# Kernel optimization log

Hardware: AMD Instinct MI355X
Metric: run time of the kernel (lower is better)

Reference implementation:

```python
import jax, jax.numpy as jnp
import numpy as np

HEADS = 6
K = 3       # kernel_size
PAD = 1     # padding (stride = 1, so AvgPool is identity and h=H, w=W)


def setup_inputs() -> dict:
    key = jax.random.key(0)
    ks = jax.random.split(key, 6)
    B, H, W, C = 8, 56, 56, 192
    k4h = (K ** 4) * HEADS  # 486
    s = 0.02
    return {
        "x":  jax.random.normal(ks[0], (B, H, W, C), jnp.float32),
        # weights stored as (in, out), i.e. transpose of torch nn.Linear.weight
        "Wv": jax.random.normal(ks[1], (C, C), jnp.float32) * s,
        "Wa": jax.random.normal(ks[2], (C, k4h), jnp.float32) * s,
        "ba": jnp.zeros((k4h,), jnp.float32),
        "Wp": jax.random.normal(ks[3], (C, C), jnp.float32) * s,
        "bp": jnp.zeros((C,), jnp.float32),
    }


def _outlook(x, Wv, Wa, ba, Wp, bp):
    B, H, W, C = x.shape
    hd = C // HEADS
    scale = hd ** (-0.5)
    k2 = K * K
    hw = H * W

    # v projection (no bias), to NCHW
    v = jnp.einsum("bhwc,cd->bdhw", x, Wv)                       # [B,C,H,W]

    # unfold: extract k x k local windows (same ordering as nn.Unfold: C, ki, kj)
    vp = jnp.pad(v, ((0, 0), (0, 0), (PAD, PAD), (PAD, PAD)))
    patches = jnp.stack(
        [vp[:, :, i:i + H, j:j + W] for i in range(K) for j in range(K)],
        axis=2,
    )                                                            # [B,C,k2,H,W]
    v = patches.reshape(B, HEADS, hd, k2, hw).transpose(0, 1, 4, 3, 2)  # [B,h,hw,k2,hd]

    # attention weights: dense predicted per location (pool is identity, stride=1)
    a = x.reshape(B, hw, C) @ Wa + ba                            # [B,hw,heads*k2*k2]
    a = a.reshape(B, hw, HEADS, k2, k2).transpose(0, 2, 1, 3, 4)  # [B,h,hw,k2,k2]
    a = jax.nn.softmax(a * scale, axis=-1)

    out = jnp.einsum("bnpkq,bnpqd->bnpkd", a, v)                 # [B,h,hw,k2,hd]

    # fold (col2im): scatter-add overlapping windows back, stride=1
    cols = out.transpose(0, 1, 4, 3, 2).reshape(B, C, K, K, H, W)
    acc = jnp.zeros((B, C, H + 2 * PAD, W + 2 * PAD), x.dtype)
    for i in range(K):
        for j in range(K):
            acc = acc.at[:, :, i:i + H, j:j + W].add(cols[:, :, i, j])
    y = acc[:, :, PAD:PAD + H, PAD:PAD + W].transpose(0, 2, 3, 1)  # [B,H,W,C]

    return y @ Wp + bp


def reference(x, Wv, Wa, ba, Wp, bp):
    return _outlook(x, Wv, Wa, ba, Wp, bp)
```

## Files before the change

### kernel.cpp

```cpp
#include <hip/hip_runtime.h>
#include <hip/hip_bf16.h>
#include <cstdint>

#define DI __device__ __forceinline__

typedef __attribute__((ext_vector_type(8))) short short8;
typedef __attribute__((ext_vector_type(4))) float f32x4;

DI float bflo(uint32_t u) { return __builtin_bit_cast(float, (uint32_t)(u << 16)); }
DI float bfhi(uint32_t u) { return __builtin_bit_cast(float, (uint32_t)(u & 0xffff0000u)); }
DI uint32_t cvtpk(float lo, float hi) {
    uint32_t r;
    asm("v_cvt_pk_bf16_f32 %0, %1, %2" : "=v"(r) : "v"(lo), "v"(hi));
    return r;
}
#if __has_builtin(__builtin_amdgcn_cvt_pk_fp8_f32)
DI uint32_t fp8pk(float a, float b) {
    return (uint32_t)__builtin_amdgcn_cvt_pk_fp8_f32(a, b, 0, false);
}
#else
DI uint32_t fp8pk(float a, float b) {
    uint32_t r;
    asm("v_cvt_pk_fp8_f32 %0, %1, %2" : "=v"(r) : "v"(a), "v"(b));
    return r;
}
#endif
#if __has_builtin(__builtin_amdgcn_cvt_f32_fp8)
#define FP8DEC(dw, sel) __builtin_amdgcn_cvt_f32_fp8((dw), (sel))
#else
DI float fp8dec_(uint32_t dw, int sel) {
    const uint32_t u = (dw >> (8 * sel)) & 0xFFu;
    const uint32_t s = (u & 0x80u) << 24;
    const uint32_t em = u & 0x7Fu;
    float mag;
    if (em >= 8) mag = __builtin_bit_cast(float, (((em >> 3) + 120u) << 23) | ((em & 7u) << 20));
    else         mag = (float)em * 0.001953125f;
    return __builtin_bit_cast(float, s | __builtin_bit_cast(uint32_t, mag));
}
#define FP8DEC(dw, sel) fp8dec_((dw), (sel))
#endif
DI void gload16(const void* g, void* s) {
    __builtin_amdgcn_global_load_lds(
        (const __attribute__((address_space(1))) uint32_t*)g,
        (__attribute__((address_space(3))) uint32_t*)s, 16, 0, 0);
}
DI int xcd_swizzle(int orig, int nwg) {
    const int q = nwg >> 3, r = nwg & 7;
    const int x = orig & 7, i = orig >> 3;
    return (x < r ? x * (q + 1) : r * (q + 1) + (x - r) * q) + i;
}

constexpr int BATCH = 8, HH_IMG = 56, WW_IMG = 56, C = 192;
constexpr int HEADS = 6, HD = 32, NA = 486;
constexpr int NAPB = 576;
constexpr int HSTA = 96;
constexpr int MROWS = BATCH * HH_IMG * WW_IMG;
constexpr int KK = 192;
constexpr int TILE_B  = 49152;
constexpr int PANEL_B = 49152;
constexpr int WTB_B   = 73728;

__global__ __launch_bounds__(256) void prep_all(const float* __restrict__ x,
                                                const float* __restrict__ Wv,
                                                const float* __restrict__ Wa,
                                                const float* __restrict__ Wp,
                                                const float* __restrict__ ba,
                                                uint8_t* __restrict__ xbf,
                                                uint8_t* __restrict__ WT,
                                                uint8_t* __restrict__ WTB,
                                                float* __restrict__ baP) {
    const int bid = blockIdx.x;
    if (bid < 2352) {
        const int g = bid * 256 + threadIdx.x;
        const int m = g / 24, cc = g % 24;
        const int ks = cc >> 2, lg = cc & 3;
        const float* src = x + (size_t)m * KK + cc * 8;
        const float4 v0 = *(const float4*)src;
        const float4 v1 = *(const float4*)(src + 4);
        uint4 o;
        o.x = cvtpk(v0.x, v0.y); o.y = cvtpk(v0.z, v0.w);
        o.z = cvtpk(v1.x, v1.y); o.w = cvtpk(v1.z, v1.w);
        const size_t off = (size_t)(m >> 7) * PANEL_B +
                           ((((m >> 4) & 7) * 6 + ks) * 64 + (lg << 4) + (m & 15)) * 16;
        *(uint4*)(xbf + off) = o;
        return;
    }
    const int tid = (bid - 2352) * 256 + threadIdx.x;
    if (tid < 18432) {
        const int s = tid % 24, rem = tid / 24;
        const int p = rem & 127, tile = rem >> 7;
        const int lc = (p >> 5) * 32 + 2 * (p & 15) + ((p >> 4) & 1);
        const int u  = tile * 128 + lc;
        const float* src = nullptr; int nc = 0, col = 0;
        if (u < 192) { src = Wv; nc = 192; col = u; }
        else {
            const int up = u - 192;
            const int head = up / HSTA, r96 = up - head * HSTA;
            if (r96 < 81) { src = Wa; nc = NA; col = head * 81 + r96; }
        }
        const int k0 = s * 8;
        uint32_t d[4];
#pragma unroll
        for (int e = 0; e < 4; ++e) {
            const float f0 = src ? src[(size_t)(k0 + 2 * e) * nc + col]     : 0.f;
            const float f1 = src ? src[(size_t)(k0 + 2 * e + 1) * nc + col] : 0.f;
            d[e] = cvtpk(f0, f1);
        }
        const int sb = (s * 16) ^ ((p & 7) << 4);
        *(uint4*)(WT + (size_t)tile * TILE_B + p * 384 + sb) =
            make_uint4(d[0], d[1], d[2], d[3]);
    } else if (tid < 18432 + 4608) {
        const int g = tid - 18432;
        const int l = g & 63, gg = g >> 6;
        const int ks = gg % 6, nrIdx = gg / 6;
        const int pp = nrIdx >> 1, h = nrIdx & 1;
        const int col = pp * 32 + 2 * (l & 15) + h;
        const int k0  = ks * 32 + (l >> 4) * 8;
        uint32_t d[4];
#pragma unroll
        for (int e = 0; e < 4; ++e) {
            const float f0 = Wp[(size_t)(k0 + 2 * e) * 192 + col];
            const float f1 = Wp[(size_t)(k0 + 2 * e + 1) * 192 + col];
            d[e] = cvtpk(f0, f1);
        }
        *(uint4*)(WTB + (size_t)g * 16) = make_uint4(d[0], d[1], d[2], d[3]);
    } else if (tid < 18432 + 4608 + NAPB) {
        const int pc = tid - 18432 - 4608;
        const int head = pc / HSTA, r96 = pc - head * HSTA;
        baP[pc] = (r96 < 81) ? ba[head * 81 + r96] : 0.f;
    }
}

__global__ __launch_bounds__(256, 2) void gemm_fr(
    const uint8_t* __restrict__ Afr,
    const uint8_t* __restrict__ WT,
    uint16_t* __restrict__ zOut, uint8_t* __restrict__ alogP,
    const float* __restrict__ baP) {
    __shared__ __align__(16) uint8_t sm[TILE_B];
    const int t    = threadIdx.x;
    const int wgid = xcd_swizzle(blockIdx.x, gridDim.x);
    const int mg   = wgid / 6, ti = wgid - mg * 6;
    const int m0   = mg * 128;
    const int l    = t & 63, wid = t >> 6;
    const int wr   = wid >> 1, wc = wid & 1;
    const int lr   = l & 15, lg = l >> 4;

    const uint8_t* wt = WT + (size_t)ti * TILE_B;
#pragma unroll
    for (int i = 0; i < 12; ++i) {
        const int off = wid * 12288 + i * 1024;
        gload16(wt + off + l * 16, sm + off);
    }

    const uint8_t* ap = Afr + (size_t)mg * PANEL_B;
    short8 aR[6][4];
#pragma unroll
    for (int ks = 0; ks < 6; ++ks)
#pragma unroll
        for (int mr = 0; mr < 4; ++mr) {
            const int r = wr * 4 + mr;
            aR[ks][mr] = *(const short8*)(ap + (size_t)(((r * 6 + ks) * 64) + l) * 16);
        }
    __syncthreads();

    f32x4 acc[4][4];
#pragma unroll
    for (int mr = 0; mr < 4; ++mr)
#pragma unroll
        for (int nr = 0; nr < 4; ++nr) acc[mr][nr] = f32x4{0.f, 0.f, 0.f, 0.f};
#pragma unroll
    for (int ks = 0; ks < 6; ++ks) {
        const int cb = ks * 64 + lg * 16;
        short8 b[4];
#pragma unroll
        for (int nr = 0; nr < 4; ++nr) {
            const int rn = wc * 64 + nr * 16 + lr;
            b[nr] = *(const short8*)(sm + rn * 384 + (cb ^ ((rn & 7) << 4)));
        }
#pragma unroll
        for (int mr = 0; mr < 4; ++mr)
#pragma unroll
            for (int nr = 0; nr < 4; ++nr)
                acc[mr][nr] = __builtin_amdgcn_mfma_f32_16x16x32_bf16(
                    aR[ks][mr], b[nr], acc[mr][nr], 0, 0, 0);
    }

    const int gcol0 = ti * 128 + wc * 64;
#pragma unroll
    for (int pr = 0; pr < 2; ++pr) {
        const int uc = gcol0 + pr * 32 + 2 * lr;
        if (uc < 192) {
#pragma unroll
            for (int mr = 0; mr < 4; ++mr) {
                const size_t rb = (size_t)(m0 + wr * 64 + mr * 16 + lg * 4);
#pragma unroll
                for (int j = 0; j < 4; ++j)
                    *(uint32_t*)(zOut + (rb + j) * 192 + uc) =
                        cvtpk(acc[mr][2 * pr][j], acc[mr][2 * pr + 1][j]);
            }
        } else {
            const int pc = uc - 192;
            const float be = baP[pc], bo = baP[pc + 1];
#pragma unroll
            for (int mr = 0; mr < 4; ++mr) {
                const size_t rb = (size_t)(m0 + wr * 64 + mr * 16 + lg * 4);
#pragma unroll
                for (int j = 0; j < 4; ++j)
                    *(uint16_t*)(alogP + (rb + j) * NAPB + pc) =
                        (uint16_t)fp8pk(acc[mr][2 * pr][j] + be,
                                        acc[mr][2 * pr + 1][j] + bo);
            }
        }
    }
}

constexpr int TH = 4, TW = 8;
constexpr int HALO_W = TW + 4;
constexpr int HSTR = 80;
constexpr int PXSTR = HEADS * HSTR;
constexpr int VL_BYTES = 96 * PXSTR;

template <int I, int J>
DI void wincoef(const uint8_t* __restrict__ rp, float (&cw)[5][5]) {
    constexpr int OFF = (I * 3 + J) * 9, A0 = OFF & ~15, BASE = OFF - A0;
    const uint4 u0 = *(const uint4*)(rp + A0);
    const uint4 u1 = *(const uint4*)(rp + A0 + 16);
    const uint32_t dd[8] = {u0.x, u0.y, u0.z, u0.w, u1.x, u1.y, u1.z, u1.w};
    constexpr float scl2 = 0.17677669529663687f * 1.4426950408889634f;
    float w[9], s = 0.f;
#define DECQ(Q) w[Q] = __builtin_amdgcn_exp2f(                                 \
        FP8DEC(dd[(BASE + Q) >> 2], (BASE + Q) & 3) * scl2); s += w[Q];
    DECQ(0) DECQ(1) DECQ(2) DECQ(3) DECQ(4) DECQ(5) DECQ(6) DECQ(7) DECQ(8)
#undef DECQ
    const float inv = __builtin_amdgcn_rcpf(s);
#pragma unroll
    for (int qi = 0; qi < 3; ++qi)
#pragma unroll
        for (int qj = 0; qj < 3; ++qj)
            cw[qi - I + 2][qj - J + 2] += w[qi * 3 + qj] * inv;
}

__global__ __launch_bounds__(192) void attn_fused(const uint16_t* __restrict__ z,
                                                  const uint8_t* __restrict__ alogP,
                                                  const uint8_t* __restrict__ WTB,
                                                  const float* __restrict__ bp,
                                                  float* __restrict__ out) {
    __shared__ __align__(16) uint8_t smem[VL_BYTES];
    const int b   = blockIdx.z;
    const int ty0 = blockIdx.y * TH, tx0 = blockIdx.x * TW;
    const int t   = threadIdx.x;

#pragma unroll
    for (int it = 0; it < 12; ++it) {
        const int f  = t + it * 192;
        const int px = f / 24, c8 = f % 24;
        const int hy = px / HALO_W, hx = px % HALO_W;
        const int y = ty0 + hy - 2, x = tx0 + hx - 2;
        uint4 val = make_uint4(0u, 0u, 0u, 0u);
        if ((unsigned)y < HH_IMG && (unsigned)x < WW_IMG)
            val = *(const uint4*)&z[(((size_t)b * HH_IMG + y) * WW_IMG + x) * C + c8 * 8];
        *(uint4*)(smem + px * PXSTR + (c8 >> 2) * HSTR + (c8 & 3) * 16) = val;
    }

    const int n   = t % HEADS, pxl = t / HEADS;
    const int py  = pxl >> 3, px_ = pxl & 7;
    const int Py  = ty0 + py, Px = tx0 + px_;

    float cw[5][5] = {};
#define WINCALL(I_, J_)                                                        \
    {                                                                          \
        const int sy = Py - I_ + 1, sx = Px - J_ + 1;                          \
        if ((unsigned)sy < HH_IMG && (unsigned)sx < WW_IMG)                    \
            wincoef<I_, J_>(alogP +                                            \
                (((size_t)b * HH_IMG + sy) * WW_IMG + sx) * NAPB + n * HSTA,   \
                cw);                                                           \
    }
    WINCALL(0, 0) WINCALL(0, 1) WINCALL(0, 2)
    WINCALL(1, 0) WINCALL(1, 1) WINCALL(1, 2)
    WINCALL(2, 0) WINCALL(2, 1) WINCALL(2, 2)
#undef WINCALL
    __syncthreads();

    float acc[HD] = {};
#pragma unroll
    for (int dy = 0; dy < 5; ++dy)
#pragma unroll
        for (int dx = 0; dx < 5; ++dx) {
            const float wq = cw[dy][dx];
            const uint8_t* vp = smem + ((py + dy) * HALO_W + (px_ + dx)) * PXSTR + n * HSTR;
#pragma unroll
            for (int v8 = 0; v8 < 4; ++v8) {
                const uint4 raw = *(const uint4*)(vp + v8 * 16);
                const uint32_t r0 = raw.x, r1 = raw.y, r2 = raw.z, r3 = raw.w;
                acc[v8*8+0] = fmaf(wq, bflo(r0), acc[v8*8+0]);
                acc[v8*8+1] = fmaf(wq, bfhi(r0), acc[v8*8+1]);
                acc[v8*8+2] = fmaf(wq, bflo(r1), acc[v8*8+2]);
                acc[v8*8+3] = fmaf(wq, bfhi(r1), acc[v8*8+3]);
                acc[v8*8+4] = fmaf(wq, bflo(r2), acc[v8*8+4]);
                acc[v8*8+5] = fmaf(wq, bfhi(r2), acc[v8*8+5]);
                acc[v8*8+6] = fmaf(wq, bflo(r3), acc[v8*8+6]);
                acc[v8*8+7] = fmaf(wq, bfhi(r3), acc[v8*8+7]);
            }
        }
    __syncthreads();

    {
        uint8_t* pb = smem + pxl * 384;
        const int key = (pxl & 7) << 4;
#pragma unroll
        for (int g2 = 0; g2 < 4; ++g2) {
            uint4 o;
            o.x = cvtpk(acc[g2 * 8 + 0], acc[g2 * 8 + 1]);
            o.y = cvtpk(acc[g2 * 8 + 2], acc[g2 * 8 + 3]);
            o.z = cvtpk(acc[g2 * 8 + 4], acc[g2 * 8 + 5]);
            o.w = cvtpk(acc[g2 * 8 + 6], acc[g2 * 8 + 7]);
            *(uint4*)(pb + ((n * 64 + g2 * 16) ^ key)) = o;
        }
    }
    __syncthreads();

    const int l = t & 63, wid = t >> 6;
    const int lr = l & 15, lg = l >> 4;
    short8 aF[2][6];
#pragma unroll
    for (int r = 0; r < 2; ++r)
#pragma unroll
        for (int ks = 0; ks < 6; ++ks) {
            const int row = r * 16 + lr;
            aF[r][ks] = *(const short8*)(smem + row * 384 +
                          ((ks * 64 + lg * 16) ^ ((row & 7) << 4)));
        }
    f32x4 gacc[2][4];
#pragma unroll
    for (int r = 0; r < 2; ++r)
#pragma unroll
        for (int f = 0; f < 4; ++f) gacc[r][f] = f32x4{0.f, 0.f, 0.f, 0.f};
#pragma unroll
    for (int ks = 0; ks < 6; ++ks) {
        short8 bF[4];
#pragma unroll
        for (int f = 0; f < 4; ++f) {
            const int nrIdx = wid * 4 + f;
            bF[f] = *(const short8*)(WTB + (size_t)(((nrIdx * 6 + ks) * 64) + l) * 16);
        }
#pragma unroll
        for (int r = 0; r < 2; ++r)
#pragma unroll
            for (int f = 0; f < 4; ++f)
                gacc[r][f] = __builtin_amdgcn_mfma_f32_16x16x32_bf16(
                    aF[r][ks], bF[f], gacc[r][f], 0, 0, 0);
    }

#pragma unroll
    for (int pi = 0; pi < 2; ++pi) {
        const int col = wid * 64 + pi * 32 + 2 * lr;
        const float be = bp[col], bo = bp[col + 1];
#pragma unroll
        for (int r = 0; r < 2; ++r)
#pragma unroll
            for (int j = 0; j < 4; ++j) {
                const int prow = r * 16 + lg * 4 + j;
                const int gy = ty0 + (prow >> 3), gx = tx0 + (prow & 7);
                float* op = out + (((size_t)b * HH_IMG + gy) * WW_IMG + gx) * C + col;
                *(float2*)op = make_float2(gacc[r][2 * pi][j] + be,
                                           gacc[r][2 * pi + 1][j] + bo);
            }
    }
}

extern "C" void kernel_launch(void* const* d_in, const int* in_sizes, int n_in,
                              void* d_out, int out_size, void* d_ws, size_t ws_size,
                              hipStream_t stream) {
    const float* x  = (const float*)d_in[0];
    const float* Wv = (const float*)d_in[1];
    const float* Wa = (const float*)d_in[2];
    const float* ba = (const float*)d_in[3];
    const float* Wp = (const float*)d_in[4];
    const float* bp = (const float*)d_in[5];
    float* out = (float*)d_out;

    uint16_t* z     = (uint16_t*)d_ws;
    uint8_t*  alogP = (uint8_t*)(z + (size_t)MROWS * C);
    uint8_t*  xbf   = alogP + (size_t)MROWS * NAPB;
    uint8_t*  WT    = xbf + (size_t)(MROWS / 128) * PANEL_B;
    uint8_t*  WTB   = WT + 6 * (size_t)TILE_B;
    float*    baP   = (float*)(WTB + WTB_B);

    prep_all<<<2352 + 93, 256, 0, stream>>>(x, Wv, Wa, Wp, ba, xbf, WT, WTB, baP);
    gemm_fr<<<(MROWS / 128) * 6, 256, 0, stream>>>(xbf, WT, z, alogP, baP);
    attn_fused<<<dim3(WW_IMG / TW, HH_IMG / TH, BATCH), dim3(192), 0, stream>>>(
        z, alogP, WTB, bp, out);
}
```

Baseline: 56.84 us.

## Fuse x bf16 conversion into GEMM kernel, dropping the global bf16 staging buffer

Moves the fp32-to-bf16 conversion of x from the prep kernel into the projection GEMM, which now loads fp32 rows, converts them, and stages them through swizzled shared memory into registers before loading the weight tile. This removes the write and re-read of an intermediate bf16 copy of x and shrinks the prep launch to weights only. In exchange, each of the six column-tile blocks per row group re-reads and re-converts fp32 x (double the bytes per read), and the A staging and weight load are now serialised with extra barriers.

```diff
diff --git a/kernel.cpp b/kernel.cpp
--- a/kernel.cpp
+++ b/kernel.cpp
@@ -56,36 +56,17 @@
 constexpr int HSTA = 96;
 constexpr int MROWS = BATCH * HH_IMG * WW_IMG;
 constexpr int KK = 192;
-constexpr int TILE_B  = 49152;
-constexpr int PANEL_B = 49152;
-constexpr int WTB_B   = 73728;
-
-__global__ __launch_bounds__(256) void prep_all(const float* __restrict__ x,
-                                                const float* __restrict__ Wv,
+constexpr int TILE_B = 49152;
+constexpr int WTB_B  = 73728;
+
+__global__ __launch_bounds__(256) void prep_wts(const float* __restrict__ Wv,
                                                 const float* __restrict__ Wa,
                                                 const float* __restrict__ Wp,
                                                 const float* __restrict__ ba,
-                                                uint8_t* __restrict__ xbf,
                                                 uint8_t* __restrict__ WT,
                                                 uint8_t* __restrict__ WTB,
                                                 float* __restrict__ baP) {
-    const int bid = blockIdx.x;
-    if (bid < 2352) {
-        const int g = bid * 256 + threadIdx.x;
-        const int m = g / 24, cc = g % 24;
-        const int ks = cc >> 2, lg = cc & 3;
-        const float* src = x + (size_t)m * KK + cc * 8;
-        const float4 v0 = *(const float4*)src;
-        const float4 v1 = *(const float4*)(src + 4);
-        uint4 o;
-        o.x = cvtpk(v0.x, v0.y); o.y = cvtpk(v0.z, v0.w);
-        o.z = cvtpk(v1.x, v1.y); o.w = cvtpk(v1.z, v1.w);
-        const size_t off = (size_t)(m >> 7) * PANEL_B +
-                           ((((m >> 4) & 7) * 6 + ks) * 64 + (lg << 4) + (m & 15)) * 16;
-        *(uint4*)(xbf + off) = o;
-        return;
-    }
-    const int tid = (bid - 2352) * 256 + threadIdx.x;
+    const int tid = blockIdx.x * 256 + threadIdx.x;
     if (tid < 18432) {
         const int s = tid % 24, rem = tid / 24;
         const int p = rem & 127, tile = rem >> 7;
@@ -132,7 +113,7 @@
 }
 
 __global__ __launch_bounds__(256, 2) void gemm_fr(
-    const uint8_t* __restrict__ Afr,
+    const float* __restrict__ x,
     const uint8_t* __restrict__ WT,
     uint16_t* __restrict__ zOut, uint8_t* __restrict__ alogP,
     const float* __restrict__ baP) {
@@ -145,22 +126,39 @@
     const int wr   = wid >> 1, wc = wid & 1;
     const int lr   = l & 15, lg = l >> 4;
 
-    const uint8_t* wt = WT + (size_t)ti * TILE_B;
 #pragma unroll
     for (int i = 0; i < 12; ++i) {
-        const int off = wid * 12288 + i * 1024;
-        gload16(wt + off + l * 16, sm + off);
-    }
-
-    const uint8_t* ap = Afr + (size_t)mg * PANEL_B;
+        const int f = t + i * 256;
+        const int m = f / 24, cb = (f % 24) * 16;
+        const int k = cb >> 1;
+        const float4 v0 = *(const float4*)(x + (size_t)(m0 + m) * KK + k);
+        const float4 v1 = *(const float4*)(x + (size_t)(m0 + m) * KK + k + 4);
+        uint4 o;
+        o.x = cvtpk(v0.x, v0.y); o.y = cvtpk(v0.z, v0.w);
+        o.z = cvtpk(v1.x, v1.y); o.w = cvtpk(v1.z, v1.w);
+        *(uint4*)(sm + m * 384 + (cb ^ ((m & 7) << 4))) = o;
+    }
+    __syncthreads();
+
     short8 aR[6][4];
 #pragma unroll
     for (int ks = 0; ks < 6; ++ks)
 #pragma unroll
         for (int mr = 0; mr < 4; ++mr) {
-            const int r = wr * 4 + mr;
-            aR[ks][mr] = *(const short8*)(ap + (size_t)(((r * 6 + ks) * 64) + l) * 16);
-        }
+            const int row = wr * 64 + mr * 16 + lr;
+            aR[ks][mr] = *(const short8*)(sm + row * 384 +
+                          ((ks * 64 + lg * 16) ^ ((row & 7) << 4)));
+        }
+    __syncthreads();
+
+    {
+        const uint8_t* wt = WT + (size_t)ti * TILE_B;
+#pragma unroll
+        for (int i = 0; i < 12; ++i) {
+            const int off = wid * 12288 + i * 1024;
+            gload16(wt + off + l * 16, sm + off);
+        }
+    }
     __syncthreads();
 
     f32x4 acc[4][4];
@@ -381,13 +379,12 @@
 
     uint16_t* z     = (uint16_t*)d_ws;
     uint8_t*  alogP = (uint8_t*)(z + (size_t)MROWS * C);
-    uint8_t*  xbf   = alogP + (size_t)MROWS * NAPB;
-    uint8_t*  WT    = xbf + (size_t)(MROWS / 128) * PANEL_B;
+    uint8_t*  WT    = alogP + (size_t)MROWS * NAPB;
     uint8_t*  WTB   = WT + 6 * (size_t)TILE_B;
     float*    baP   = (float*)(WTB + WTB_B);
 
-    prep_all<<<2352 + 93, 256, 0, stream>>>(x, Wv, Wa, Wp, ba, xbf, WT, WTB, baP);
-    gemm_fr<<<(MROWS / 128) * 6, 256, 0, stream>>>(xbf, WT, z, alogP, baP);
+    prep_wts<<<93, 256, 0, stream>>>(Wv, Wa, Wp, ba, WT, WTB, baP);
+    gemm_fr<<<(MROWS / 128) * 6, 256, 0, stream>>>(x, WT, z, alogP, baP);
     attn_fused<<<dim3(WW_IMG / TW, HH_IMG / TH, BATCH), dim3(192), 0, stream>>>(
         z, alogP, WTB, bp, out);
 }
```

Result: slower. 58.08 us (+2.2%).
